# Performance work log

Hardware: AMD Instinct MI355X
Metric: run time of the kernel (lower is better)

## Reference

```python
import jax, jax.numpy as jnp
import numpy as np

B, N, DIM = 64, 197, 768
H = 12
IN_DIM = 768
HD = IN_DIM // H  # 64


def setup_inputs() -> dict:
    key = jax.random.key(0)
    k1, k2, k3 = jax.random.split(key, 3)
    x = jax.random.normal(k1, (B, N, DIM), dtype=jnp.float32)
    # learnable per-head scale, initialized to head_dim**-0.5
    scale = (DIM // H) ** (-0.5) * jnp.ones((H,), dtype=jnp.float32)
    w_qkv = jax.random.normal(k2, (3 * IN_DIM, DIM), dtype=jnp.float32) * 0.02  # qkv_bias=False
    w_proj = jax.random.normal(k3, (IN_DIM, IN_DIM), dtype=jnp.float32) * 0.02
    b_proj = jnp.zeros((IN_DIM,), dtype=jnp.float32)
    return {"x": x, "scale": scale, "w_qkv": w_qkv, "w_proj": w_proj, "b_proj": b_proj}


def reference(x, scale, w_qkv, w_proj, b_proj):
    Bx, Nx, C = x.shape
    # qkv projection -> [3, B, H, N, HD]
    qkv = jnp.einsum('bnc,oc->bno', x, w_qkv).reshape(Bx, Nx, 3, H, HD)
    qkv = qkv.transpose(2, 0, 3, 1, 4)
    q, k, v = qkv[0], qkv[1], qkv[2]
    # per-head learnable scale (LMSA)
    attn = jnp.einsum('bhid,bhjd->bhij', q, k) * scale[None, :, None, None]
    # diagonal mask -> -inf (self-token masking)
    diag = jnp.eye(Nx, dtype=bool)  # [N, N]
    attn = jnp.where(diag[None, None, :, :], -jnp.inf, attn)
    attn = jax.nn.softmax(attn, axis=-1)
    out = jnp.einsum('bhij,bhjd->bhid', attn, v)  # [B, H, N, HD]
    out = out.transpose(0, 2, 1, 3).reshape(Bx, Nx, IN_DIM)
    out = out @ w_proj.T + b_proj
    return out + x  # num_heads > 1 branch: residual add
```

## Files before the change

kernel.cpp:

```cpp
#include <hip/hip_runtime.h>
#include <cstdint>
#include <cstddef>

#define DEV static __device__ __forceinline__

typedef __attribute__((ext_vector_type(8))) short bf16x8;
typedef __attribute__((ext_vector_type(4))) float f32x4;

constexpr int NB   = 64;
constexpr int NTOK = 197;
constexpr int DIMC = 768;
constexpr int NH   = 12;
constexpr int HDIM = 64;
constexpr int MTOK = NB * NTOK;
constexpr int QKVO = 3 * DIMC;
constexpr int BH   = NB * NH;
constexpr int KROWS = 198;
constexpr int VTS   = 232;
constexpr int OBS   = 68;
constexpr int GM    = (MTOK + 127) / 128;
constexpr int GM64  = MTOK / 64;

DEV unsigned short f2bf(float f) {
  union { float f; uint32_t u; } v; v.f = f;
  uint32_t u = v.u;
  return (unsigned short)((u + 0x7FFFu + ((u >> 16) & 1u)) >> 16);
}

DEV uint32_t pack_bf2(float a, float b) {
  return (uint32_t)f2bf(a) | ((uint32_t)f2bf(b) << 16);
}

DEV f32x4 mfma16(bf16x8 a, bf16x8 b, f32x4 c) {
  return __builtin_amdgcn_mfma_f32_16x16x32_bf16(a, b, c, 0, 0, 0);
}

DEV void async_cp16(const unsigned short* g, unsigned short* l) {
  __builtin_amdgcn_global_load_lds(
      (__attribute__((address_space(1))) void*)g,
      (__attribute__((address_space(3))) void*)l, 16, 0, 0);
}

DEV void swizzle_idx(int lin, int gridM, int gridN, int& mt, int& nt) {
  int per = 16 * gridN;
  int sup = lin / per;
  int bm  = sup * 16;
  int Gm  = gridM - bm; if (Gm > 16) Gm = 16;
  int rem = lin - sup * per;
  nt = rem / Gm;
  mt = bm + (rem - nt * Gm);
}

constexpr int CVB1 = (MTOK * DIMC) / 4096;
constexpr int CVB2 = (QKVO * DIMC) / 4096;
constexpr int CVB3 = (DIMC * DIMC) / 4096;
constexpr int CVNB = CVB1 + CVB2 + CVB3;

__global__ void __launch_bounds__(256) cvt_all(const float* __restrict__ x,
                                               const float* __restrict__ wq,
                                               const float* __restrict__ wp,
                                               unsigned short* __restrict__ xb,
                                               unsigned short* __restrict__ wqb,
                                               unsigned short* __restrict__ wpb) {
  int blk = blockIdx.x;
  const float* s; unsigned short* d;
  if (blk < CVB1)               { s = x;  d = xb; }
  else if (blk < CVB1 + CVB2)   { s = wq; d = wqb; blk -= CVB1; }
  else                          { s = wp; d = wpb; blk -= CVB1 + CVB2; }
  size_t base = (size_t)blk * 4096 + (size_t)threadIdx.x * 4;
#pragma unroll
  for (int j = 0; j < 4; ++j) {
    size_t i = base + (size_t)j * 1024;
    float4 f = *(const float4*)(s + i);
    ushort4 o;
    o.x = f2bf(f.x); o.y = f2bf(f.y); o.z = f2bf(f.z); o.w = f2bf(f.w);
    *(ushort4*)(d + i) = o;
  }
}

__global__ void __launch_bounds__(256) gemm_qkv(const unsigned short* __restrict__ A,
                                                const unsigned short* __restrict__ Bw,
                                                unsigned short* __restrict__ qkv) {
  __shared__ __align__(16) unsigned short As[128 * 64];
  __shared__ __align__(16) unsigned short Bs[128 * 64];
  const int tid = threadIdx.x, lane = tid & 63, wave = tid >> 6;
  const int wm = wave & 1, wn = wave >> 1;
  const int l16 = lane & 15, quad = lane >> 4;
  int mt, nt;
  swizzle_idx(blockIdx.x, GM, QKVO / 128, mt, nt);
  const int mbase = mt * 128, nbase = nt * 128;

  f32x4 acc[4][4];
#pragma unroll
  for (int i = 0; i < 4; ++i)
#pragma unroll
    for (int j = 0; j < 4; ++j) acc[i][j] = {0.f, 0.f, 0.f, 0.f};

  for (int k0 = 0; k0 < DIMC; k0 += 64) {
#pragma unroll
    for (int i = 0; i < 4; ++i) {
      int c = i * 256 + tid;
      int row = c >> 3, cc = c & 7;
      int gc = (cc ^ (row & 7)) * 8;
      int ar = mbase + row; ar = ar < MTOK ? ar : MTOK - 1;
      async_cp16(A  + (size_t)ar * DIMC + k0 + gc, As + c * 8);
      async_cp16(Bw + (size_t)(nbase + row) * DIMC + k0 + gc, Bs + c * 8);
    }
    __syncthreads();
#pragma unroll
    for (int kk = 0; kk < 64; kk += 32) {
      const int cw = (kk >> 3) + quad;
      bf16x8 af[4], bfr[4];
#pragma unroll
      for (int mi = 0; mi < 4; ++mi) {
        int r = wm * 64 + mi * 16 + l16;
        af[mi] = *(const bf16x8*)(As + r * 64 + (cw ^ (r & 7)) * 8);
      }
#pragma unroll
      for (int ni = 0; ni < 4; ++ni) {
        int r = wn * 64 + ni * 16 + l16;
        bfr[ni] = *(const bf16x8*)(Bs + r * 64 + (cw ^ (r & 7)) * 8);
      }
#pragma unroll
      for (int mi = 0; mi < 4; ++mi)
#pragma unroll
        for (int ni = 0; ni < 4; ++ni)
          acc[mi][ni] = mfma16(af[mi], bfr[ni], acc[mi][ni]);
    }
    __syncthreads();
  }

  const int oc64  = nbase + wn * 64;
  const int which = oc64 / DIMC;
  const int h     = (oc64 % DIMC) / HDIM;
#pragma unroll
  for (int mi = 0; mi < 4; ++mi) {
    int t0 = mbase + wm * 64 + mi * 16 + quad * 4;
#pragma unroll
    for (int r = 0; r < 4; ++r) {
      int t = t0 + r;
      if (t < MTOK) {
        int b = t / NTOK, n = t - b * NTOK;
        size_t base = ((size_t)((which * NB + b) * NH + h) * NTOK + n) * HDIM;
#pragma unroll
        for (int ni = 0; ni < 4; ++ni)
          qkv[base + ni * 16 + l16] = f2bf(acc[mi][ni][r]);
      }
    }
  }
}

__global__ void __launch_bounds__(256) gemm_proj(const unsigned short* __restrict__ A,
                                                 const unsigned short* __restrict__ Bw,
                                                 const float* __restrict__ bias,
                                                 const float* __restrict__ xres,
                                                 float* __restrict__ out) {
  __shared__ __align__(16) unsigned short As[64 * 64];
  __shared__ __align__(16) unsigned short Bs[128 * 64];
  const int tid = threadIdx.x, lane = tid & 63, wave = tid >> 6;
  const int wm = wave & 1, wn = wave >> 1;
  const int l16 = lane & 15, quad = lane >> 4;
  int mt, nt;
  swizzle_idx(blockIdx.x, GM64, DIMC / 128, mt, nt);
  const int mbase = mt * 64, nbase = nt * 128;

  f32x4 acc[2][4];
#pragma unroll
  for (int i = 0; i < 2; ++i)
#pragma unroll
    for (int j = 0; j < 4; ++j) acc[i][j] = {0.f, 0.f, 0.f, 0.f};

  for (int k0 = 0; k0 < DIMC; k0 += 64) {
#pragma unroll
    for (int i = 0; i < 2; ++i) {
      int c = i * 256 + tid;
      int row = c >> 3, cc = c & 7;
      int gc = (cc ^ (row & 7)) * 8;
      async_cp16(A + (size_t)(mbase + row) * DIMC + k0 + gc, As + c * 8);
    }
#pragma unroll
    for (int i = 0; i < 4; ++i) {
      int c = i * 256 + tid;
      int row = c >> 3, cc = c & 7;
      int gc = (cc ^ (row & 7)) * 8;
      async_cp16(Bw + (size_t)(nbase + row) * DIMC + k0 + gc, Bs + c * 8);
    }
    __syncthreads();
#pragma unroll
    for (int kk = 0; kk < 64; kk += 32) {
      const int cw = (kk >> 3) + quad;
      bf16x8 af[2], bfr[4];
#pragma unroll
      for (int mi = 0; mi < 2; ++mi) {
        int r = wm * 32 + mi * 16 + l16;
        af[mi] = *(const bf16x8*)(As + r * 64 + (cw ^ (r & 7)) * 8);
      }
#pragma unroll
      for (int ni = 0; ni < 4; ++ni) {
        int r = wn * 64 + ni * 16 + l16;
        bfr[ni] = *(const bf16x8*)(Bs + r * 64 + (cw ^ (r & 7)) * 8);
      }
#pragma unroll
      for (int mi = 0; mi < 2; ++mi)
#pragma unroll
        for (int ni = 0; ni < 4; ++ni)
          acc[mi][ni] = mfma16(af[mi], bfr[ni], acc[mi][ni]);
    }
    __syncthreads();
  }

  const int oc = nbase + wn * 64;
#pragma unroll
  for (int mi = 0; mi < 2; ++mi) {
    int t0 = mbase + wm * 32 + mi * 16 + quad * 4;
#pragma unroll
    for (int r = 0; r < 4; ++r) {
      int t = t0 + r;
      size_t rowb = (size_t)t * DIMC;
#pragma unroll
      for (int ni = 0; ni < 4; ++ni) {
        int o = oc + ni * 16 + l16;
        out[rowb + o] = acc[mi][ni][r] + bias[o] + xres[rowb + o];
      }
    }
  }
}

__global__ void __launch_bounds__(256, 2) attn_fused(const unsigned short* __restrict__ qkv,
                                                     const float* __restrict__ scale,
                                                     unsigned short* __restrict__ aout) {
  __shared__ __align__(16) unsigned short Ks[KROWS * 64];
  __shared__ __align__(16) unsigned short Vt[HDIM * VTS];
  __shared__ __align__(16) unsigned short Ob[4 * 16 * OBS];

  const int tid = threadIdx.x, lane = tid & 63, wave = tid >> 6;
  const int l16 = lane & 15, quad = lane >> 4;
  const int bh = blockIdx.x;
  const int b = bh / NH, h = bh - b * NH;

  const unsigned short* qg = qkv + (size_t)bh * (NTOK * HDIM);
  const unsigned short* kg = qkv + (size_t)(BH + bh) * (NTOK * HDIM);
  const unsigned short* vg = qkv + (size_t)(2 * BH + bh) * (NTOK * HDIM);
  const float sc = scale[h];

#pragma unroll
  for (int i = 0; i < 7; ++i) {
    int c = i * 256 + tid;
    if (c < KROWS * 8) {
      int row = c >> 3, cc = c & 7;
      async_cp16(kg + (size_t)row * 64 + ((cc ^ (row & 7)) * 8), Ks + c * 8);
    }
  }
  {
    const int dcol = tid & 63;
    const int slab = tid >> 6;
#pragma unroll
    for (int p = 0; p < 7; ++p) {
      int n0 = p * 32 + slab * 8;
      union { unsigned short us[8]; bf16x8 v; } tr;
#pragma unroll
      for (int i = 0; i < 8; ++i) {
        int n = n0 + i; n = n > NTOK - 1 ? NTOK - 1 : n;
        tr.us[i] = vg[(size_t)n * HDIM + dcol];
      }
      *(bf16x8*)(Vt + dcol * VTS + n0) = tr.v;
    }
  }
  __syncthreads();

  const int srcA  = l16 + ((quad & 1) << 5);
  const int srcB  = srcA + 16;
  const int stsel = quad >> 1;
  unsigned short* ob = Ob + wave * (16 * OBS);

  for (int mt = wave; mt < 13; mt += 4) {
    int qr = mt * 16 + l16; if (qr > NTOK - 1) qr = NTOK - 1;
    bf16x8 qb0 = *(const bf16x8*)(qg + (size_t)qr * 64 + quad * 8);
    bf16x8 qb1 = *(const bf16x8*)(qg + (size_t)qr * 64 + 32 + quad * 8);
    const int mg = mt * 16 + l16;

    f32x4 s[7][2];
#pragma unroll
    for (int jc = 0; jc < 7; ++jc)
#pragma unroll
      for (int st = 0; st < 2; ++st) {
        if (jc == 6 && st == 1) { s[6][1] = {0.f, 0.f, 0.f, 0.f}; continue; }
        int jrow = (jc * 2 + st) * 16 + l16;
        jrow = jrow > NTOK ? NTOK : jrow;
        const unsigned short* kr = Ks + jrow * 64;
        bf16x8 ka0 = *(const bf16x8*)(kr + (quad       ^ (jrow & 7)) * 8);
        bf16x8 ka1 = *(const bf16x8*)(kr + ((4 + quad) ^ (jrow & 7)) * 8);
        f32x4 t = {0.f, 0.f, 0.f, 0.f};
        t = mfma16(ka0, qb0, t);
        t = mfma16(ka1, qb1, t);
        s[jc][st] = t;
      }

    float cmax = -1e30f;
#pragma unroll
    for (int jc = 0; jc < 7; ++jc)
#pragma unroll
      for (int st = 0; st < 2; ++st)
#pragma unroll
        for (int r = 0; r < 4; ++r) {
          int jg = jc * 32 + st * 16 + quad * 4 + r;
          float v = s[jc][st][r] * sc;
          v = (jg >= NTOK || jg == mg) ? -1e30f : v;
          s[jc][st][r] = v;
          cmax = fmaxf(cmax, v);
        }
    cmax = fmaxf(cmax, __shfl_xor(cmax, 16));
    cmax = fmaxf(cmax, __shfl_xor(cmax, 32));
    float psum = 0.f;
#pragma unroll
    for (int jc = 0; jc < 7; ++jc)
#pragma unroll
      for (int st = 0; st < 2; ++st)
#pragma unroll
        for (int r = 0; r < 4; ++r) {
          float e = __expf(s[jc][st][r] - cmax);
          psum += e;
          s[jc][st][r] = e;
        }
    psum += __shfl_xor(psum, 16);
    psum += __shfl_xor(psum, 32);
    const float inv = 1.0f / psum;

    f32x4 oacc[4];
#pragma unroll
    for (int dt = 0; dt < 4; ++dt) oacc[dt] = {0.f, 0.f, 0.f, 0.f};

#pragma unroll
    for (int jc = 0; jc < 7; ++jc) {
      uint32_t u0 = pack_bf2(s[jc][0][0], s[jc][0][1]);
      uint32_t v0 = pack_bf2(s[jc][0][2], s[jc][0][3]);
      uint32_t u1 = pack_bf2(s[jc][1][0], s[jc][1][1]);
      uint32_t v1 = pack_bf2(s[jc][1][2], s[jc][1][3]);
      uint32_t au0 = (uint32_t)__shfl((int)u0, srcA);
      uint32_t av0 = (uint32_t)__shfl((int)v0, srcA);
      uint32_t au1 = (uint32_t)__shfl((int)u1, srcA);
      uint32_t av1 = (uint32_t)__shfl((int)v1, srcA);
      uint32_t bu0 = (uint32_t)__shfl((int)u0, srcB);
      uint32_t bv0 = (uint32_t)__shfl((int)v0, srcB);
      uint32_t bu1 = (uint32_t)__shfl((int)u1, srcB);
      uint32_t bv1 = (uint32_t)__shfl((int)v1, srcB);
      union { uint32_t u[4]; bf16x8 v; } pb;
      pb.u[0] = stsel ? au1 : au0;
      pb.u[1] = stsel ? av1 : av0;
      pb.u[2] = stsel ? bu1 : bu0;
      pb.u[3] = stsel ? bv1 : bv0;
#pragma unroll
      for (int dt = 0; dt < 4; ++dt) {
        bf16x8 va = *(const bf16x8*)(Vt + (dt * 16 + l16) * VTS +
                                     jc * 32 + quad * 8);
        oacc[dt] = mfma16(va, pb.v, oacc[dt]);
      }
    }

#pragma unroll
    for (int dt = 0; dt < 4; ++dt) {
      ushort4 pk;
      pk.x = f2bf(oacc[dt][0] * inv);
      pk.y = f2bf(oacc[dt][1] * inv);
      pk.z = f2bf(oacc[dt][2] * inv);
      pk.w = f2bf(oacc[dt][3] * inv);
      *(ushort4*)(ob + l16 * OBS + dt * 16 + quad * 4) = pk;
    }
    __asm__ __volatile__("s_waitcnt lgkmcnt(0)" ::: "memory");
#pragma unroll
    for (int rnd = 0; rnd < 4; ++rnd) {
      int q   = rnd * 4 + (lane >> 4);
      int o8  = lane & 15;
      uint2 d8 = *(const uint2*)(ob + q * OBS + o8 * 4);
      int qrow = mt * 16 + q;
      if (qrow < NTOK) {
        size_t obase = (size_t)(b * NTOK + qrow) * DIMC + h * HDIM;
        *(uint2*)(aout + obase + o8 * 4) = d8;
      }
    }
  }
}

extern "C" void kernel_launch(void* const* d_in, const int* in_sizes, int n_in,
                              void* d_out, int out_size, void* d_ws, size_t ws_size,
                              hipStream_t stream) {
  const float* x     = (const float*)d_in[0];
  const float* scale = (const float*)d_in[1];
  const float* wqkv  = (const float*)d_in[2];
  const float* wproj = (const float*)d_in[3];
  const float* bproj = (const float*)d_in[4];
  float* out = (float*)d_out;

  unsigned short* xb   = (unsigned short*)d_ws;
  unsigned short* wqb  = xb  + (size_t)MTOK * DIMC;
  unsigned short* wpb  = wqb + (size_t)QKVO * DIMC;
  unsigned short* qkvb = wpb + (size_t)DIMC * DIMC;
  unsigned short* attb = xb;

  cvt_all<<<CVNB, 256, 0, stream>>>(x, wqkv, wproj, xb, wqb, wpb);
  gemm_qkv<<<GM * (QKVO / 128), 256, 0, stream>>>(xb, wqb, qkvb);
  attn_fused<<<BH, 256, 0, stream>>>(qkvb, scale, attb);
  gemm_proj<<<GM64 * (DIMC / 128), 256, 0, stream>>>(attb, wpb, bproj, x, out);
}
```

Measured before the change: 216.4 us.

## Rewrite QKV GEMM as 256x256 double-buffered ping-pong pipeline with 8 waves

The QKV projection GEMM moves from 128x128 tiles with a synchronous load/compute loop to 256x256 tiles over 512 threads. It uses double-buffered dynamic LDS (128KB) and quarter-tile staged async loads that are interleaved with four MFMA phases. Explicit barriers, waitcnt and setprio control the schedule. The aim is to hide global-to-LDS latency and raise data reuse per tile, at the cost of larger LDS and register use and fewer blocks, which may hurt occupancy and leave partial tiles in the ragged M dimension.

```diff
diff --git a/kernel.cpp b/kernel.cpp
--- a/kernel.cpp
+++ b/kernel.cpp
@@ -18,8 +18,14 @@
 constexpr int KROWS = 198;
 constexpr int VTS   = 232;
 constexpr int OBS   = 68;
-constexpr int GM    = (MTOK + 127) / 128;
 constexpr int GM64  = MTOK / 64;
+
+constexpr int BM2  = 256;
+constexpr int BN2  = 256;
+constexpr int GM2  = (MTOK + BM2 - 1) / BM2;
+constexpr int GN2  = QKVO / BN2;
+constexpr int NKT  = DIMC / 64;
+constexpr int BUFH = 32768;
 
 DEV unsigned short f2bf(float f) {
   union { float f; uint32_t u; } v; v.f = f;
@@ -78,64 +84,142 @@
   }
 }
 
-__global__ void __launch_bounds__(256) gemm_qkv(const unsigned short* __restrict__ A,
-                                                const unsigned short* __restrict__ Bw,
-                                                unsigned short* __restrict__ qkv) {
-  __shared__ __align__(16) unsigned short As[128 * 64];
-  __shared__ __align__(16) unsigned short Bs[128 * 64];
+DEV void stage_A_qm(const unsigned short* A, unsigned short* lds,
+                    int mbase, int k0, int qm, int tid) {
+#pragma unroll
+  for (int u = 0; u < 2; ++u) {
+    int c = u * 512 + tid;
+    int row = c >> 3, cc = c & 7;
+    int arow = qm * 64 + (row & 63) + ((row >> 6) << 7);
+    int gr = mbase + arow; gr = gr < MTOK ? gr : MTOK - 1;
+    int gc = (cc ^ (arow & 7)) * 8;
+    async_cp16(A + (size_t)gr * DIMC + k0 + gc, lds + arow * 64 + cc * 8);
+  }
+}
+
+DEV void stage_B_qn(const unsigned short* Bw, unsigned short* lds,
+                    int nbase, int k0, int qn, int tid) {
+#pragma unroll
+  for (int u = 0; u < 2; ++u) {
+    int c = u * 512 + tid;
+    int row = c >> 3, cc = c & 7;
+    int brow = (row >> 5) * 64 + qn * 32 + (row & 31);
+    int gc = (cc ^ (brow & 7)) * 8;
+    async_cp16(Bw + (size_t)(nbase + brow) * DIMC + k0 + gc, lds + brow * 64 + cc * 8);
+  }
+}
+
+template <int QM>
+DEV void ldA(const unsigned short* Ac, int wm, int l16, int quad, bf16x8 (&af)[4][2]) {
+#pragma unroll
+  for (int mi = 0; mi < 4; ++mi)
+#pragma unroll
+    for (int kk = 0; kk < 2; ++kk) {
+      int r = wm * 128 + QM * 64 + mi * 16 + l16;
+      af[mi][kk] = *(const bf16x8*)(Ac + r * 64 + (((kk * 4 + quad) ^ (r & 7)) * 8));
+    }
+}
+
+template <int QN>
+DEV void ldB(const unsigned short* Bc, int wn, int l16, int quad, bf16x8 (&bf_)[2][2]) {
+#pragma unroll
+  for (int ni = 0; ni < 2; ++ni)
+#pragma unroll
+    for (int kk = 0; kk < 2; ++kk) {
+      int r = wn * 64 + QN * 32 + ni * 16 + l16;
+      bf_[ni][kk] = *(const bf16x8*)(Bc + r * 64 + (((kk * 4 + quad) ^ (r & 7)) * 8));
+    }
+}
+
+template <int QM, int QN>
+DEV void ph_mfma(bf16x8 (&af)[4][2], bf16x8 (&bf_)[2][2], f32x4 (&acc)[8][4]) {
+  __builtin_amdgcn_s_setprio(1);
+#pragma unroll
+  for (int kk = 0; kk < 2; ++kk)
+#pragma unroll
+    for (int mi = 0; mi < 4; ++mi)
+#pragma unroll
+      for (int ni = 0; ni < 2; ++ni)
+        acc[QM * 4 + mi][QN * 2 + ni] =
+            mfma16(af[mi][kk], bf_[ni][kk], acc[QM * 4 + mi][QN * 2 + ni]);
+  __builtin_amdgcn_s_setprio(0);
+}
+
+__global__ void __launch_bounds__(512, 2) gemm_qkv(const unsigned short* __restrict__ A,
+                                                   const unsigned short* __restrict__ Bw,
+                                                   unsigned short* __restrict__ qkv) {
+  extern __shared__ unsigned short lds[];
   const int tid = threadIdx.x, lane = tid & 63, wave = tid >> 6;
   const int wm = wave & 1, wn = wave >> 1;
   const int l16 = lane & 15, quad = lane >> 4;
   int mt, nt;
-  swizzle_idx(blockIdx.x, GM, QKVO / 128, mt, nt);
-  const int mbase = mt * 128, nbase = nt * 128;
-
-  f32x4 acc[4][4];
-#pragma unroll
-  for (int i = 0; i < 4; ++i)
+  swizzle_idx(blockIdx.x, GM2, GN2, mt, nt);
+  const int mbase = mt * BM2, nbase = nt * BN2;
+
+  f32x4 acc[8][4];
+#pragma unroll
+  for (int i = 0; i < 8; ++i)
 #pragma unroll
     for (int j = 0; j < 4; ++j) acc[i][j] = {0.f, 0.f, 0.f, 0.f};
 
-  for (int k0 = 0; k0 < DIMC; k0 += 64) {
-#pragma unroll
-    for (int i = 0; i < 4; ++i) {
-      int c = i * 256 + tid;
-      int row = c >> 3, cc = c & 7;
-      int gc = (cc ^ (row & 7)) * 8;
-      int ar = mbase + row; ar = ar < MTOK ? ar : MTOK - 1;
-      async_cp16(A  + (size_t)ar * DIMC + k0 + gc, As + c * 8);
-      async_cp16(Bw + (size_t)(nbase + row) * DIMC + k0 + gc, Bs + c * 8);
-    }
-    __syncthreads();
-#pragma unroll
-    for (int kk = 0; kk < 64; kk += 32) {
-      const int cw = (kk >> 3) + quad;
-      bf16x8 af[4], bfr[4];
-#pragma unroll
-      for (int mi = 0; mi < 4; ++mi) {
-        int r = wm * 64 + mi * 16 + l16;
-        af[mi] = *(const bf16x8*)(As + r * 64 + (cw ^ (r & 7)) * 8);
-      }
-#pragma unroll
-      for (int ni = 0; ni < 4; ++ni) {
-        int r = wn * 64 + ni * 16 + l16;
-        bfr[ni] = *(const bf16x8*)(Bs + r * 64 + (cw ^ (r & 7)) * 8);
-      }
-#pragma unroll
-      for (int mi = 0; mi < 4; ++mi)
-#pragma unroll
-        for (int ni = 0; ni < 4; ++ni)
-          acc[mi][ni] = mfma16(af[mi], bfr[ni], acc[mi][ni]);
-    }
-    __syncthreads();
+  unsigned short* A0 = lds;
+  unsigned short* B0 = lds + 16384;
+  unsigned short* A1 = lds + BUFH;
+  unsigned short* B1 = lds + BUFH + 16384;
+
+  stage_A_qm(A, A0, mbase, 0, 0, tid);
+  stage_B_qn(Bw, B0, nbase, 0, 0, tid);
+  stage_A_qm(A, A0, mbase, 0, 1, tid);
+  stage_B_qn(Bw, B0, nbase, 0, 1, tid);
+  stage_A_qm(A, A1, mbase, 64, 0, tid);
+  stage_B_qn(Bw, B1, nbase, 64, 0, tid);
+  asm volatile("s_waitcnt vmcnt(4)" ::: "memory");
+  __builtin_amdgcn_s_barrier();
+
+  bf16x8 af[4][2], b0[2][2], b1[2][2];
+
+  for (int kt = 0; kt < NKT; ++kt) {
+    unsigned short* Ac = (kt & 1) ? A1 : A0;
+    unsigned short* Bc = (kt & 1) ? B1 : B0;
+    unsigned short* An = (kt & 1) ? A0 : A1;
+    unsigned short* Bn = (kt & 1) ? B0 : B1;
+
+    ldA<0>(Ac, wm, l16, quad, af);
+    ldB<0>(Bc, wn, l16, quad, b0);
+    if (kt < NKT - 1) stage_A_qm(A, An, mbase, (kt + 1) * 64, 1, tid);
+    __builtin_amdgcn_s_barrier();
+    ph_mfma<0, 0>(af, b0, acc);
+    asm volatile("s_waitcnt lgkmcnt(0)" ::: "memory");
+    __builtin_amdgcn_s_barrier();
+
+    ldB<1>(Bc, wn, l16, quad, b1);
+    if (kt < NKT - 1) stage_B_qn(Bw, Bn, nbase, (kt + 1) * 64, 1, tid);
+    __builtin_amdgcn_s_barrier();
+    ph_mfma<0, 1>(af, b1, acc);
+    asm volatile("s_waitcnt lgkmcnt(0)" ::: "memory");
+    __builtin_amdgcn_s_barrier();
+
+    ldA<1>(Ac, wm, l16, quad, af);
+    if (kt < NKT - 2) stage_A_qm(A, Ac, mbase, (kt + 2) * 64, 0, tid);
+    __builtin_amdgcn_s_barrier();
+    ph_mfma<1, 0>(af, b0, acc);
+    asm volatile("s_waitcnt lgkmcnt(0)" ::: "memory");
+    __builtin_amdgcn_s_barrier();
+
+    if (kt < NKT - 2) stage_B_qn(Bw, Bc, nbase, (kt + 2) * 64, 0, tid);
+    __builtin_amdgcn_s_barrier();
+    ph_mfma<1, 1>(af, b1, acc);
+    if (kt >= NKT - 2) asm volatile("s_waitcnt vmcnt(0) lgkmcnt(0)" ::: "memory");
+    else               asm volatile("s_waitcnt vmcnt(4) lgkmcnt(0)" ::: "memory");
+    __builtin_amdgcn_s_barrier();
   }
 
   const int oc64  = nbase + wn * 64;
   const int which = oc64 / DIMC;
   const int h     = (oc64 % DIMC) / HDIM;
 #pragma unroll
-  for (int mi = 0; mi < 4; ++mi) {
-    int t0 = mbase + wm * 64 + mi * 16 + quad * 4;
+  for (int mi8 = 0; mi8 < 8; ++mi8) {
+    int t0 = mbase + wm * 128 + mi8 * 16 + quad * 4;
 #pragma unroll
     for (int r = 0; r < 4; ++r) {
       int t = t0 + r;
@@ -144,7 +228,7 @@
         size_t base = ((size_t)((which * NB + b) * NH + h) * NTOK + n) * HDIM;
 #pragma unroll
         for (int ni = 0; ni < 4; ++ni)
-          qkv[base + ni * 16 + l16] = f2bf(acc[mi][ni][r]);
+          qkv[base + ni * 16 + l16] = f2bf(acc[mi8][ni][r]);
       }
     }
   }
@@ -397,8 +481,15 @@
   unsigned short* qkvb = wpb + (size_t)DIMC * DIMC;
   unsigned short* attb = xb;
 
+  static bool qkv_attr_set = false;
+  if (!qkv_attr_set) {
+    hipFuncSetAttribute(reinterpret_cast<const void*>(gemm_qkv),
+                        hipFuncAttributeMaxDynamicSharedMemorySize, 131072);
+    qkv_attr_set = true;
+  }
+
   cvt_all<<<CVNB, 256, 0, stream>>>(x, wqkv, wproj, xb, wqb, wpb);
-  gemm_qkv<<<GM * (QKVO / 128), 256, 0, stream>>>(xb, wqb, qkvb);
+  gemm_qkv<<<GM2 * GN2, 512, 131072, stream>>>(xb, wqb, qkvb);
   attn_fused<<<BH, 256, 0, stream>>>(qkvb, scale, attb);
   gemm_proj<<<GM64 * (DIMC / 128), 256, 0, stream>>>(attb, wpb, bproj, x, out);
 }
```

Result: faster. 211.2 us (-2.4%).

## Enlarge QKV GEMM to 256x256 tiles with double-buffered LDS pipeline

Applied to the files above, without the earlier changes.

The QKV projection GEMM moves from 128x128 tiles with 256 threads to 256x256 tiles with 1024 threads (16 waves). It uses 128KB of dynamic LDS split into two buffers, so the next K panel loads while the current one is multiplied. Alternate wave rows process the two K halves in opposite order, and MFMA sections are wrapped in setprio. The aim is more data reuse per tile and hidden global-load latency, at the cost of fewer, larger blocks, waves on the last M tile, and one block per CU because of the LDS size.

```diff
diff --git a/kernel.cpp b/kernel.cpp
--- a/kernel.cpp
+++ b/kernel.cpp
@@ -18,8 +18,14 @@
 constexpr int KROWS = 198;
 constexpr int VTS   = 232;
 constexpr int OBS   = 68;
-constexpr int GM    = (MTOK + 127) / 128;
 constexpr int GM64  = MTOK / 64;
+
+constexpr int BM2  = 256;
+constexpr int BN2  = 256;
+constexpr int GM2  = (MTOK + BM2 - 1) / BM2;
+constexpr int GN2  = QKVO / BN2;
+constexpr int NKT  = DIMC / 64;
+constexpr int BUFH = 32768;
 
 DEV unsigned short f2bf(float f) {
   union { float f; uint32_t u; } v; v.f = f;
@@ -78,17 +84,55 @@
   }
 }
 
-__global__ void __launch_bounds__(256) gemm_qkv(const unsigned short* __restrict__ A,
-                                                const unsigned short* __restrict__ Bw,
-                                                unsigned short* __restrict__ qkv) {
-  __shared__ __align__(16) unsigned short As[128 * 64];
-  __shared__ __align__(16) unsigned short Bs[128 * 64];
+DEV void stage_panel(const unsigned short* src, unsigned short* dst,
+                     int rbase, int k0, int clampR, int tid) {
+#pragma unroll
+  for (int u = 0; u < 2; ++u) {
+    int c = u * 1024 + tid;
+    int row = c >> 3, cc = c & 7;
+    int gr = rbase + row; gr = gr < clampR ? gr : clampR - 1;
+    int gc = (cc ^ (row & 7)) * 8;
+    async_cp16(src + (size_t)gr * DIMC + k0 + gc, dst + c * 8);
+  }
+}
+
+template <int KK>
+DEV void ldAB(const unsigned short* Ac, const unsigned short* Bc,
+              int wm, int wn, int l16, int quad,
+              bf16x8 (&af)[4], bf16x8 (&bf_)[4]) {
+#pragma unroll
+  for (int mi = 0; mi < 4; ++mi) {
+    int r = wm * 64 + mi * 16 + l16;
+    af[mi] = *(const bf16x8*)(Ac + r * 64 + (((KK * 4 + quad) ^ (r & 7)) * 8));
+  }
+#pragma unroll
+  for (int ni = 0; ni < 4; ++ni) {
+    int r = wn * 64 + ni * 16 + l16;
+    bf_[ni] = *(const bf16x8*)(Bc + r * 64 + (((KK * 4 + quad) ^ (r & 7)) * 8));
+  }
+}
+
+DEV void mm16(bf16x8 (&af)[4], bf16x8 (&bf_)[4], f32x4 (&acc)[4][4]) {
+  __builtin_amdgcn_s_setprio(1);
+#pragma unroll
+  for (int mi = 0; mi < 4; ++mi)
+#pragma unroll
+    for (int ni = 0; ni < 4; ++ni)
+      acc[mi][ni] = mfma16(af[mi], bf_[ni], acc[mi][ni]);
+  __builtin_amdgcn_s_setprio(0);
+}
+
+__global__ void __launch_bounds__(1024, 4) gemm_qkv(const unsigned short* __restrict__ A,
+                                                    const unsigned short* __restrict__ Bw,
+                                                    unsigned short* __restrict__ qkv) {
+  extern __shared__ unsigned short lds[];
   const int tid = threadIdx.x, lane = tid & 63, wave = tid >> 6;
-  const int wm = wave & 1, wn = wave >> 1;
+  const int wm = wave >> 2, wn = wave & 3;
   const int l16 = lane & 15, quad = lane >> 4;
+  const int stag = wm & 1;
   int mt, nt;
-  swizzle_idx(blockIdx.x, GM, QKVO / 128, mt, nt);
-  const int mbase = mt * 128, nbase = nt * 128;
+  swizzle_idx(blockIdx.x, GM2, GN2, mt, nt);
+  const int mbase = mt * BM2, nbase = nt * BN2;
 
   f32x4 acc[4][4];
 #pragma unroll
@@ -96,38 +140,45 @@
 #pragma unroll
     for (int j = 0; j < 4; ++j) acc[i][j] = {0.f, 0.f, 0.f, 0.f};
 
-  for (int k0 = 0; k0 < DIMC; k0 += 64) {
-#pragma unroll
-    for (int i = 0; i < 4; ++i) {
-      int c = i * 256 + tid;
-      int row = c >> 3, cc = c & 7;
-      int gc = (cc ^ (row & 7)) * 8;
-      int ar = mbase + row; ar = ar < MTOK ? ar : MTOK - 1;
-      async_cp16(A  + (size_t)ar * DIMC + k0 + gc, As + c * 8);
-      async_cp16(Bw + (size_t)(nbase + row) * DIMC + k0 + gc, Bs + c * 8);
-    }
-    __syncthreads();
-#pragma unroll
-    for (int kk = 0; kk < 64; kk += 32) {
-      const int cw = (kk >> 3) + quad;
-      bf16x8 af[4], bfr[4];
-#pragma unroll
-      for (int mi = 0; mi < 4; ++mi) {
-        int r = wm * 64 + mi * 16 + l16;
-        af[mi] = *(const bf16x8*)(As + r * 64 + (cw ^ (r & 7)) * 8);
-      }
-#pragma unroll
-      for (int ni = 0; ni < 4; ++ni) {
-        int r = wn * 64 + ni * 16 + l16;
-        bfr[ni] = *(const bf16x8*)(Bs + r * 64 + (cw ^ (r & 7)) * 8);
-      }
-#pragma unroll
-      for (int mi = 0; mi < 4; ++mi)
-#pragma unroll
-        for (int ni = 0; ni < 4; ++ni)
-          acc[mi][ni] = mfma16(af[mi], bfr[ni], acc[mi][ni]);
-    }
-    __syncthreads();
+  unsigned short* A0 = lds;
+  unsigned short* B0 = lds + 16384;
+  unsigned short* A1 = lds + BUFH;
+  unsigned short* B1 = lds + BUFH + 16384;
+
+  stage_panel(A,  A0, mbase, 0, MTOK, tid);
+  stage_panel(Bw, B0, nbase, 0, QKVO, tid);
+  asm volatile("s_waitcnt vmcnt(0)" ::: "memory");
+  __builtin_amdgcn_s_barrier();
+
+  for (int kt = 0; kt < NKT; ++kt) {
+    const unsigned short* Ac = (kt & 1) ? A1 : A0;
+    const unsigned short* Bc = (kt & 1) ? B1 : B0;
+    unsigned short* An = (kt & 1) ? A0 : A1;
+    unsigned short* Bn = (kt & 1) ? B0 : B1;
+
+    if (kt + 1 < NKT) {
+      int k0n = (kt + 1) * 64;
+      stage_panel(A,  An, mbase, k0n, MTOK, tid);
+      stage_panel(Bw, Bn, nbase, k0n, QKVO, tid);
+    }
+
+    bf16x8 af[4], bf_[4];
+    if (stag == 0) {
+      ldAB<0>(Ac, Bc, wm, wn, l16, quad, af, bf_);
+      mm16(af, bf_, acc);
+      ldAB<1>(Ac, Bc, wm, wn, l16, quad, af, bf_);
+      mm16(af, bf_, acc);
+    } else {
+      ldAB<1>(Ac, Bc, wm, wn, l16, quad, af, bf_);
+      mm16(af, bf_, acc);
+      ldAB<0>(Ac, Bc, wm, wn, l16, quad, af, bf_);
+      mm16(af, bf_, acc);
+    }
+
+    if (kt + 1 < NKT) {
+      asm volatile("s_waitcnt vmcnt(0)" ::: "memory");
+      __builtin_amdgcn_s_barrier();
+    }
   }
 
   const int oc64  = nbase + wn * 64;
@@ -397,8 +448,15 @@
   unsigned short* qkvb = wpb + (size_t)DIMC * DIMC;
   unsigned short* attb = xb;
 
+  static bool qkv_attr_set = false;
+  if (!qkv_attr_set) {
+    hipFuncSetAttribute(reinterpret_cast<const void*>(gemm_qkv),
+                        hipFuncAttributeMaxDynamicSharedMemorySize, 131072);
+    qkv_attr_set = true;
+  }
+
   cvt_all<<<CVNB, 256, 0, stream>>>(x, wqkv, wproj, xb, wqb, wpb);
-  gemm_qkv<<<GM * (QKVO / 128), 256, 0, stream>>>(xb, wqb, qkvb);
+  gemm_qkv<<<GM2 * GN2, 1024, 131072, stream>>>(xb, wqb, qkvb);
   attn_fused<<<BH, 256, 0, stream>>>(qkvb, scale, attb);
   gemm_proj<<<GM64 * (DIMC / 128), 256, 0, stream>>>(attb, wpb, bproj, x, out);
 }
```

After: 228.4 us. 5.5% more time.
